# Performance work log

Measured on AMD Instinct MI355X. Metric: run time of the kernel, lower is better.

## Reference

```python
import jax, jax.numpy as jnp
import numpy as np

D = 1024  # input_dim


def setup_inputs() -> dict:
    key = jax.random.key(0)
    ks = jax.random.split(key, 7)
    s = 1.0 / np.sqrt(D)
    return {
        "x": jax.random.normal(ks[0], (4, 2048, D), dtype=jnp.float32),
        "wq": jax.random.normal(ks[1], (D, D), dtype=jnp.float32) * s,
        "bq": jax.random.normal(ks[2], (D,), dtype=jnp.float32) * s,
        "wk": jax.random.normal(ks[3], (D, D), dtype=jnp.float32) * s,
        "bk": jax.random.normal(ks[4], (D,), dtype=jnp.float32) * s,
        "wv": jax.random.normal(ks[5], (D, D), dtype=jnp.float32) * s,
        "bv": jax.random.normal(ks[6], (D,), dtype=jnp.float32) * s,
    }


def reference(x, wq, bq, wk, bk, wv, bv):
    # torch Linear: y = x @ W^T + b
    q = jnp.einsum('btd,ed->bte', x, wq) + bq  # (B,T,D)
    k = jnp.einsum('btd,ed->bte', x, wk) + bk
    v = jnp.einsum('btd,ed->bte', x, wv) + bv
    scale = 1.0 / jnp.sqrt(jnp.asarray(D, dtype=x.dtype))
    scores = jnp.einsum('btd,bsd->bts', q, k) * scale  # (B,T,T)
    attn = jax.nn.softmax(scores, axis=-1)
    return jnp.einsum('bts,bsd->btd', attn, v)
```

## Files before the change

kernel.cpp:

```cpp
#include <hip/hip_runtime.h>
#include <stdint.h>

#define BB 4
#define TT 2048
#define DD 1024

typedef unsigned short u16;
typedef unsigned int u32;
typedef u16 u16x4 __attribute__((ext_vector_type(4)));
typedef u16 u16x8 __attribute__((ext_vector_type(8)));
typedef float f32x4 __attribute__((ext_vector_type(4)));
typedef short s16x8 __attribute__((ext_vector_type(8)));

__device__ __forceinline__ u16 f2bf(float f) {
  u32 u = __float_as_uint(f);
  return (u16)((u + 0x7fffu + ((u >> 16) & 1u)) >> 16);
}
__device__ __forceinline__ float bf2f(u16 h) {
  return __uint_as_float((u32)h << 16);
}

__device__ __forceinline__ void gload_lds16(const void* g, void* l) {
  __builtin_amdgcn_global_load_lds(
      (const __attribute__((address_space(1))) u32*)g,
      (__attribute__((address_space(3))) u32*)l, 16, 0, 0);
}

__device__ __forceinline__ void swz(int BMv, int BNv, int& tileM, int& tileN) {
  const int gN = gridDim.x, gM = gridDim.y;
  const int L = blockIdx.y * gN + blockIdx.x;
  const int xcd = L & 7, j = L >> 3;
  const int Mq = gM >> 2, Nq = gN >> 1;
  tileM = (((xcd >> 1) * Mq) + j / Nq) * BMv;
  tileN = (((xcd & 1) * Nq) + j % Nq) * BNv;
}

__global__ __launch_bounds__(256) void cast_bf16_kernel(
    const float* __restrict__ in, u16* __restrict__ out, int n8) {
  int i = blockIdx.x * 256 + threadIdx.x;
  if (i >= n8) return;
  const f32x4* p = (const f32x4*)in;
  f32x4 a = p[2 * (size_t)i];
  f32x4 b = p[2 * (size_t)i + 1];
  u16x8 o;
  o[0] = f2bf(a[0]); o[1] = f2bf(a[1]); o[2] = f2bf(a[2]); o[3] = f2bf(a[3]);
  o[4] = f2bf(b[0]); o[5] = f2bf(b[1]); o[6] = f2bf(b[2]); o[7] = f2bf(b[3]);
  *(u16x8*)(out + 8 * (size_t)i) = o;
}

__global__ __launch_bounds__(256) void wcast_kernel(
    const float* __restrict__ wq, const float* __restrict__ wk,
    const float* __restrict__ wv, u16* __restrict__ out) {
  int i = blockIdx.x * 256 + threadIdx.x;
  const int n1 = DD * DD / 8;
  const float* src = i < n1 ? wq : (i < 2 * n1 ? wk : wv);
  int ii = i < n1 ? i : (i < 2 * n1 ? i - n1 : i - 2 * n1);
  const f32x4* p = (const f32x4*)src;
  f32x4 a = p[2 * (size_t)ii];
  f32x4 b = p[2 * (size_t)ii + 1];
  u16x8 o;
  o[0] = f2bf(a[0]); o[1] = f2bf(a[1]); o[2] = f2bf(a[2]); o[3] = f2bf(a[3]);
  o[4] = f2bf(b[0]); o[5] = f2bf(b[1]); o[6] = f2bf(b[2]); o[7] = f2bf(b[3]);
  *(u16x8*)(out + 8 * (size_t)i) = o;
}

__global__ __launch_bounds__(256) void bias_concat_kernel(
    const float* __restrict__ bq, const float* __restrict__ bk,
    const float* __restrict__ bv, float* __restrict__ out) {
  int i = blockIdx.x * 256 + threadIdx.x;
  float v = i < DD ? bq[i] : (i < 2 * DD ? bk[i - DD] : bv[i - 2 * DD]);
  out[i] = v;
}

template <int NR>
__device__ __forceinline__ void kloop256(
    const u16* __restrict__ A, const u16* __restrict__ B, int lda, int ldb,
    int K, int tileM, int tileN, u16* sm, f32x4 (&acc)[8][NR]) {
  constexpr int AE = 16384;
  constexpr int BUF = AE + NR * 4096;
  const int tid = threadIdx.x;
  const int lane = tid & 63;
  const int wave = tid >> 6;
  const int quad = lane >> 4;
  const int l15 = lane & 15;
  const int wm = (wave >> 2) << 7;
  const int wn = (wave & 3) * (NR * 16);

  const int chl = wave * 64 + lane;
  const int rloc = chl >> 3;
  const int cg = ((chl & 7) ^ (rloc & 7)) * 8;
  const int ldst = chl * 8;

  const u16* gA[4];
  const u16* gB[NR];
#pragma unroll
  for (int j = 0; j < 4; ++j)
    gA[j] = A + (size_t)(tileM + j * 64 + rloc) * lda + cg;
#pragma unroll
  for (int j = 0; j < NR; ++j)
    gB[j] = B + (size_t)(tileN + j * 64 + rloc) * ldb + cg;

  const int x0 = (quad ^ (l15 & 7)) * 8;
  int aOff[8];
  int bOff[NR];
#pragma unroll
  for (int i = 0; i < 8; ++i) aOff[i] = (wm + i * 16 + l15) * 64 + x0;
#pragma unroll
  for (int i = 0; i < NR; ++i) bOff[i] = AE + (wn + i * 16 + l15) * 64 + x0;

  {
    u16* d = sm;
    gload_lds16(gA[0], d + 0 * 4096 + ldst);
    gload_lds16(gA[2], d + 2 * 4096 + ldst);
#pragma unroll
    for (int j = 0; j < NR; ++j) gload_lds16(gB[j], d + AE + j * 4096 + ldst);
    gload_lds16(gA[1], d + 1 * 4096 + ldst);
    gload_lds16(gA[3], d + 3 * 4096 + ldst);
#pragma unroll
    for (int j = 0; j < 4; ++j) gA[j] += 64;
#pragma unroll
    for (int j = 0; j < NR; ++j) gB[j] += 64;
  }
  asm volatile("s_waitcnt vmcnt(2)" ::: "memory");
  __builtin_amdgcn_s_barrier();
  __builtin_amdgcn_sched_barrier(0);

  const int NT = K >> 6;
  for (int t = 0; t < NT; ++t) {
    const u16* sb = sm + (t & 1) * BUF;
    u16* st = sm + ((t + 1) & 1) * BUF;
    const bool stg = (t + 1 < NT);
    s16x8 af[4], bf[NR];

#pragma unroll
    for (int i = 0; i < 4; ++i) af[i] = *(const s16x8*)(sb + aOff[i]);
#pragma unroll
    for (int i = 0; i < NR; ++i) bf[i] = *(const s16x8*)(sb + bOff[i]);
    if (stg) {
      gload_lds16(gA[0], st + 0 * 4096 + ldst);
      gload_lds16(gA[2], st + 2 * 4096 + ldst);
    }
    __builtin_amdgcn_s_barrier();
    __builtin_amdgcn_sched_barrier(0);
    asm volatile("s_waitcnt lgkmcnt(0)" ::: "memory");
    __builtin_amdgcn_s_setprio(1);
#pragma unroll
    for (int mi = 0; mi < 4; ++mi)
#pragma unroll
      for (int ni = 0; ni < NR; ++ni)
        acc[mi][ni] = __builtin_amdgcn_mfma_f32_16x16x32_bf16(
            af[mi], bf[ni], acc[mi][ni], 0, 0, 0);
    __builtin_amdgcn_s_setprio(0);
    if (stg) {
      asm volatile("s_waitcnt vmcnt(2)" ::: "memory");
    } else {
      asm volatile("s_waitcnt vmcnt(0)" ::: "memory");
    }
    __builtin_amdgcn_s_barrier();
    __builtin_amdgcn_sched_barrier(0);

#pragma unroll
    for (int i = 0; i < 4; ++i) af[i] = *(const s16x8*)(sb + aOff[4 + i]);
    if (stg) {
      gload_lds16(gB[0], st + AE + 0 * 4096 + ldst);
      gload_lds16(gB[1], st + AE + 1 * 4096 + ldst);
    }
    __builtin_amdgcn_s_barrier();
    __builtin_amdgcn_sched_barrier(0);
    asm volatile("s_waitcnt lgkmcnt(0)" ::: "memory");
    __builtin_amdgcn_s_setprio(1);
#pragma unroll
    for (int mi = 0; mi < 4; ++mi)
#pragma unroll
      for (int ni = 0; ni < NR; ++ni)
        acc[4 + mi][ni] = __builtin_amdgcn_mfma_f32_16x16x32_bf16(
            af[mi], bf[ni], acc[4 + mi][ni], 0, 0, 0);
    __builtin_amdgcn_s_setprio(0);
    __builtin_amdgcn_s_barrier();
    __builtin_amdgcn_sched_barrier(0);

#pragma unroll
    for (int i = 0; i < 4; ++i) af[i] = *(const s16x8*)(sb + (aOff[i] ^ 32));
#pragma unroll
    for (int i = 0; i < NR; ++i) bf[i] = *(const s16x8*)(sb + (bOff[i] ^ 32));
    if (stg) {
      gload_lds16(gB[2], st + AE + 2 * 4096 + ldst);
      if constexpr (NR == 4) gload_lds16(gB[3], st + AE + 3 * 4096 + ldst);
    }
    __builtin_amdgcn_s_barrier();
    __builtin_amdgcn_sched_barrier(0);
    asm volatile("s_waitcnt lgkmcnt(0)" ::: "memory");
    __builtin_amdgcn_s_setprio(1);
#pragma unroll
    for (int mi = 0; mi < 4; ++mi)
#pragma unroll
      for (int ni = 0; ni < NR; ++ni)
        acc[mi][ni] = __builtin_amdgcn_mfma_f32_16x16x32_bf16(
            af[mi], bf[ni], acc[mi][ni], 0, 0, 0);
    __builtin_amdgcn_s_setprio(0);
    __builtin_amdgcn_s_barrier();
    __builtin_amdgcn_sched_barrier(0);

#pragma unroll
    for (int i = 0; i < 4; ++i)
      af[i] = *(const s16x8*)(sb + (aOff[4 + i] ^ 32));
    if (stg) {
      gload_lds16(gA[1], st + 1 * 4096 + ldst);
      gload_lds16(gA[3], st + 3 * 4096 + ldst);
#pragma unroll
      for (int j = 0; j < 4; ++j) gA[j] += 64;
#pragma unroll
      for (int j = 0; j < NR; ++j) gB[j] += 64;
    }
    __builtin_amdgcn_s_barrier();
    __builtin_amdgcn_sched_barrier(0);
    asm volatile("s_waitcnt lgkmcnt(0)" ::: "memory");
    __builtin_amdgcn_s_setprio(1);
#pragma unroll
    for (int mi = 0; mi < 4; ++mi)
#pragma unroll
      for (int ni = 0; ni < NR; ++ni)
        acc[4 + mi][ni] = __builtin_amdgcn_mfma_f32_16x16x32_bf16(
            af[mi], bf[ni], acc[4 + mi][ni], 0, 0, 0);
    __builtin_amdgcn_s_setprio(0);
    if (stg) asm volatile("s_waitcnt vmcnt(2)" ::: "memory");
    __builtin_amdgcn_s_barrier();
    __builtin_amdgcn_sched_barrier(0);
  }
}

__device__ __forceinline__ void kloop_bt(
    const u16* __restrict__ A, const u16* __restrict__ B, int lda, int ldb,
    int K, int tileM, int tileN, u16* sA, u16* sB, f32x4 acc[4][4]) {
  const int tid = threadIdx.x;
  const int lane = tid & 63;
  const int wave = tid >> 6;
  const int quad = lane >> 4;
  const int l15 = lane & 15;
  const int wm = (wave >> 1) << 6;
  const int wn = (wave & 1) << 6;

  const u16 *gA[4], *gB[4];
  u16 *lA[4], *lB[4];
#pragma unroll
  for (int j = 0; j < 4; ++j) {
    const int ch = wave * 256 + j * 64 + lane;
    const int r = ch >> 3;
    const int cg = ((ch & 7) ^ (r & 7)) * 8;
    gA[j] = A + (size_t)(tileM + r) * lda + cg;
    gB[j] = B + (size_t)(tileN + r) * ldb + cg;
    lA[j] = sA + wave * 2048 + j * 512;
    lB[j] = sB + wave * 2048 + j * 512;
  }

  const int x0 = (quad ^ (l15 & 7)) * 8;
  int aOff[4], bOff[4];
#pragma unroll
  for (int i = 0; i < 4; ++i) {
    aOff[i] = (wm + i * 16 + l15) * 64 + x0;
    bOff[i] = (wn + i * 16 + l15) * 64 + x0;
  }

  for (int it = 0; it < K; it += 64) {
#pragma unroll
    for (int j = 0; j < 4; ++j) gload_lds16(gA[j], lA[j]);
#pragma unroll
    for (int j = 0; j < 4; ++j) gload_lds16(gB[j], lB[j]);
#pragma unroll
    for (int j = 0; j < 4; ++j) { gA[j] += 64; gB[j] += 64; }
    __syncthreads();

    s16x8 af[4], bf[4];
#pragma unroll
    for (int i = 0; i < 4; ++i) af[i] = *(const s16x8*)(sA + aOff[i]);
#pragma unroll
    for (int i = 0; i < 4; ++i) bf[i] = *(const s16x8*)(sB + bOff[i]);
#pragma unroll
    for (int mi = 0; mi < 4; ++mi)
#pragma unroll
      for (int ni = 0; ni < 4; ++ni)
        acc[mi][ni] = __builtin_amdgcn_mfma_f32_16x16x32_bf16(
            af[mi], bf[ni], acc[mi][ni], 0, 0, 0);

#pragma unroll
    for (int i = 0; i < 4; ++i) af[i] = *(const s16x8*)(sA + (aOff[i] ^ 32));
#pragma unroll
    for (int i = 0; i < 4; ++i) bf[i] = *(const s16x8*)(sB + (bOff[i] ^ 32));
#pragma unroll
    for (int mi = 0; mi < 4; ++mi)
#pragma unroll
      for (int ni = 0; ni < 4; ++ni)
        acc[mi][ni] = __builtin_amdgcn_mfma_f32_16x16x32_bf16(
            af[mi], bf[ni], acc[mi][ni], 0, 0, 0);
    __syncthreads();
  }
}

__global__ __launch_bounds__(512, 2) void gemm_qkv(
    const u16* __restrict__ A, const u16* __restrict__ B,
    u16* __restrict__ qk, u16* __restrict__ vt, const float* __restrict__ bias) {
  __shared__ u16 sm[2 * (16384 + 3 * 4096)];
  const int lane = threadIdx.x & 63;
  const int wave = threadIdx.x >> 6;
  const int quad = lane >> 4;
  const int l15 = lane & 15;
  const int wm = (wave >> 2) << 7;
  const int wn = (wave & 3) * 48;
  int tileM, tileN;
  swz(256, 192, tileM, tileN);

  f32x4 acc[8][3] = {};
  kloop256<3>(A, B, DD, DD, DD, tileM, tileN, sm, acc);

  const int rowB = tileM + wm + quad * 4;
#pragma unroll
  for (int ni = 0; ni < 3; ++ni) {
    const int c0 = tileN + wn + ni * 16;
    const int col = c0 + l15;
    const float bs = bias[col];
    if (c0 < 2048) {
      const float scale = c0 < 1024 ? 0.03125f : 1.0f;
#pragma unroll
      for (int mi = 0; mi < 8; ++mi)
#pragma unroll
        for (int r = 0; r < 4; ++r)
          qk[(size_t)(rowB + mi * 16 + r) * 2048 + col] =
              f2bf((acc[mi][ni][r] + bs) * scale);
    } else {
      const int b = tileM >> 11;
      const int tBase = rowB & 2047;
      u16* vb = vt + (size_t)b * DD * TT + (size_t)(col - 2048) * TT;
#pragma unroll
      for (int mi = 0; mi < 8; ++mi) {
        u16x4 o;
#pragma unroll
        for (int r = 0; r < 4; ++r) o[r] = f2bf(acc[mi][ni][r] + bs);
        *(u16x4*)(vb + tBase + mi * 16) = o;
      }
    }
  }
}

__global__ __launch_bounds__(512, 2) void gemm_s(
    const u16* __restrict__ qk, u16* __restrict__ sbuf,
    float* __restrict__ part) {
  __shared__ u16 sm[2 * (16384 + 4 * 4096)];
  const int lane = threadIdx.x & 63;
  const int wave = threadIdx.x >> 6;
  const int quad = lane >> 4;
  const int l15 = lane & 15;
  const int wm = (wave >> 2) << 7;
  const int wn = (wave & 3) << 6;
  int tileM, tileN;
  swz(256, 256, tileM, tileN);
  const int z = blockIdx.z;

  const u16* A = qk + (size_t)z * TT * 2048;
  const u16* B = qk + (size_t)z * TT * 2048 + 1024;

  f32x4 acc[8][4] = {};
  kloop256<4>(A, B, 2048, 2048, 1024, tileM, tileN, sm, acc);

  const int rowB = tileM + wm + quad * 4;
  const int colB = tileN + wn + l15;
  u16* C = sbuf + (size_t)z * TT * 2048;
  const int nIdx2 = (tileN + wn) >> 6;
  float* prow = part + ((size_t)z * 32 + nIdx2) * TT;
#pragma unroll
  for (int mi = 0; mi < 8; ++mi)
#pragma unroll
    for (int r = 0; r < 4; ++r) {
      const int row = rowB + mi * 16 + r;
      u16* crow = C + (size_t)row * 2048 + colB;
      float s = 0.f;
#pragma unroll
      for (int ni = 0; ni < 4; ++ni) {
        const u16 h = f2bf(__expf(acc[mi][ni][r]));
        crow[ni * 16] = h;
        s += bf2f(h);
      }
#pragma unroll
      for (int m = 1; m <= 8; m <<= 1) s += __shfl_xor(s, m, 64);
      if (l15 == 0) prow[row] = s;
    }
}

__global__ __launch_bounds__(256, 2) void gemm_pv(
    const u16* __restrict__ sbuf, const u16* __restrict__ vt,
    float* __restrict__ out, const float* __restrict__ part) {
  __shared__ u16 sA[128 * 64];
  __shared__ u16 sB[128 * 64];
  __shared__ float rowInv[128];
  const int tid = threadIdx.x;
  const int lane = tid & 63;
  const int wave = tid >> 6;
  const int quad = lane >> 4;
  const int l15 = lane & 15;
  const int wm = (wave >> 1) << 6;
  const int wn = (wave & 1) << 6;
  int tileM, tileN;
  swz(128, 128, tileM, tileN);
  const int z = blockIdx.z;

  if (tid < 128) {
    const float* pp = part + (size_t)z * 32 * TT + tileM + tid;
    float s = 0.f;
#pragma unroll
    for (int j = 0; j < 32; ++j) s += pp[j * TT];
    rowInv[tid] = 1.0f / s;
  }

  const u16* A = sbuf + (size_t)z * TT * 2048;
  const u16* B = vt + (size_t)z * DD * TT;

  f32x4 acc[4][4] = {};
  kloop_bt(A, B, 2048, TT, TT, tileM, tileN, sA, sB, acc);

  const int rowB = tileM + wm + quad * 4;
  const int colB = tileN + wn + l15;
  float* C = out + (size_t)z * TT * DD;
#pragma unroll
  for (int mi = 0; mi < 4; ++mi)
#pragma unroll
    for (int r = 0; r < 4; ++r) {
      const int lrow = wm + quad * 4 + mi * 16 + r;
      const float inv = rowInv[lrow];
      float* crow = C + (size_t)(rowB + mi * 16 + r) * DD + colB;
#pragma unroll
      for (int ni = 0; ni < 4; ++ni) crow[ni * 16] = acc[mi][ni][r] * inv;
    }
}

extern "C" void kernel_launch(void* const* d_in, const int* in_sizes, int n_in,
                              void* d_out, int out_size, void* d_ws,
                              size_t ws_size, hipStream_t stream) {
  const float* x = (const float*)d_in[0];
  const float* wq = (const float*)d_in[1];
  const float* bq = (const float*)d_in[2];
  const float* wk = (const float*)d_in[3];
  const float* bk = (const float*)d_in[4];
  const float* wv = (const float*)d_in[5];
  const float* bv = (const float*)d_in[6];
  float* out = (float*)d_out;

  const size_t MB = 1024 * 1024;
  if (ws_size < 103 * MB) return;
  char* ws = (char*)d_ws;
  u16* xbf = (u16*)(ws);
  float* part = (float*)(ws);
  u16* wcat = (u16*)(ws + 16 * MB);
  float* bcat = (float*)(ws + 22 * MB);
  u16* qk = (u16*)(ws + 23 * MB);
  u16* vt = (u16*)(ws + 55 * MB);
  u16* sbuf = (u16*)(ws + 71 * MB);

  const dim3 blk256(256);
  const dim3 blk512(512);

  cast_bf16_kernel<<<BB * TT * DD / 8 / 256, blk256, 0, stream>>>(
      x, xbf, BB * TT * DD / 8);
  wcast_kernel<<<3 * DD * DD / 8 / 256, blk256, 0, stream>>>(wq, wk, wv, wcat);
  bias_concat_kernel<<<12, blk256, 0, stream>>>(bq, bk, bv, bcat);

  gemm_qkv<<<dim3(3 * DD / 192, BB * TT / 256, 1), blk512, 0, stream>>>(
      xbf, wcat, qk, vt, bcat);

  gemm_s<<<dim3(TT / 256, TT / 256, BB), blk512, 0, stream>>>(qk, sbuf, part);

  gemm_pv<<<dim3(DD / 128, TT / 128, BB), blk256, 0, stream>>>(
      sbuf, vt, out, part);
}
```

Before: 240.5 us.

## Front-load global-to-LDS prefetch in GEMM loop and stage QK epilogue through LDS

After: 238.1 us. Within noise of the previous version (-1.0%).

```diff
diff --git a/kernel.cpp b/kernel.cpp
--- a/kernel.cpp
+++ b/kernel.cpp
@@ -139,10 +139,13 @@
     if (stg) {
       gload_lds16(gA[0], st + 0 * 4096 + ldst);
       gload_lds16(gA[2], st + 2 * 4096 + ldst);
+      gload_lds16(gB[0], st + AE + 0 * 4096 + ldst);
+      gload_lds16(gB[1], st + AE + 1 * 4096 + ldst);
     }
     __builtin_amdgcn_s_barrier();
     __builtin_amdgcn_sched_barrier(0);
     asm volatile("s_waitcnt lgkmcnt(0)" ::: "memory");
+    __builtin_amdgcn_sched_barrier(0);
     __builtin_amdgcn_s_setprio(1);
 #pragma unroll
     for (int mi = 0; mi < 4; ++mi)
@@ -152,7 +155,7 @@
             af[mi], bf[ni], acc[mi][ni], 0, 0, 0);
     __builtin_amdgcn_s_setprio(0);
     if (stg) {
-      asm volatile("s_waitcnt vmcnt(2)" ::: "memory");
+      asm volatile("s_waitcnt vmcnt(4)" ::: "memory");
     } else {
       asm volatile("s_waitcnt vmcnt(0)" ::: "memory");
     }
@@ -162,12 +165,19 @@
 #pragma unroll
     for (int i = 0; i < 4; ++i) af[i] = *(const s16x8*)(sb + aOff[4 + i]);
     if (stg) {
-      gload_lds16(gB[0], st + AE + 0 * 4096 + ldst);
-      gload_lds16(gB[1], st + AE + 1 * 4096 + ldst);
+      if constexpr (NR >= 3) gload_lds16(gB[2], st + AE + 2 * 4096 + ldst);
+      if constexpr (NR >= 4) gload_lds16(gB[3], st + AE + 3 * 4096 + ldst);
+      gload_lds16(gA[1], st + 1 * 4096 + ldst);
+      gload_lds16(gA[3], st + 3 * 4096 + ldst);
+#pragma unroll
+      for (int j = 0; j < 4; ++j) gA[j] += 64;
+#pragma unroll
+      for (int j = 0; j < NR; ++j) gB[j] += 64;
     }
     __builtin_amdgcn_s_barrier();
     __builtin_amdgcn_sched_barrier(0);
     asm volatile("s_waitcnt lgkmcnt(0)" ::: "memory");
+    __builtin_amdgcn_sched_barrier(0);
     __builtin_amdgcn_s_setprio(1);
 #pragma unroll
     for (int mi = 0; mi < 4; ++mi)
@@ -183,13 +193,10 @@
     for (int i = 0; i < 4; ++i) af[i] = *(const s16x8*)(sb + (aOff[i] ^ 32));
 #pragma unroll
     for (int i = 0; i < NR; ++i) bf[i] = *(const s16x8*)(sb + (bOff[i] ^ 32));
-    if (stg) {
-      gload_lds16(gB[2], st + AE + 2 * 4096 + ldst);
-      if constexpr (NR == 4) gload_lds16(gB[3], st + AE + 3 * 4096 + ldst);
-    }
     __builtin_amdgcn_s_barrier();
     __builtin_amdgcn_sched_barrier(0);
     asm volatile("s_waitcnt lgkmcnt(0)" ::: "memory");
+    __builtin_amdgcn_sched_barrier(0);
     __builtin_amdgcn_s_setprio(1);
 #pragma unroll
     for (int mi = 0; mi < 4; ++mi)
@@ -204,17 +211,10 @@
 #pragma unroll
     for (int i = 0; i < 4; ++i)
       af[i] = *(const s16x8*)(sb + (aOff[4 + i] ^ 32));
-    if (stg) {
-      gload_lds16(gA[1], st + 1 * 4096 + ldst);
-      gload_lds16(gA[3], st + 3 * 4096 + ldst);
-#pragma unroll
-      for (int j = 0; j < 4; ++j) gA[j] += 64;
-#pragma unroll
-      for (int j = 0; j < NR; ++j) gB[j] += 64;
-    }
     __builtin_amdgcn_s_barrier();
     __builtin_amdgcn_sched_barrier(0);
     asm volatile("s_waitcnt lgkmcnt(0)" ::: "memory");
+    __builtin_amdgcn_sched_barrier(0);
     __builtin_amdgcn_s_setprio(1);
 #pragma unroll
     for (int mi = 0; mi < 4; ++mi)
@@ -300,8 +300,9 @@
     const u16* __restrict__ A, const u16* __restrict__ B,
     u16* __restrict__ qk, u16* __restrict__ vt, const float* __restrict__ bias) {
   __shared__ u16 sm[2 * (16384 + 3 * 4096)];
-  const int lane = threadIdx.x & 63;
-  const int wave = threadIdx.x >> 6;
+  const int tid = threadIdx.x;
+  const int lane = tid & 63;
+  const int wave = tid >> 6;
   const int quad = lane >> 4;
   const int l15 = lane & 15;
   const int wm = (wave >> 2) << 7;
@@ -312,24 +313,25 @@
   f32x4 acc[8][3] = {};
   kloop256<3>(A, B, DD, DD, DD, tileM, tileN, sm, acc);
 
-  const int rowB = tileM + wm + quad * 4;
+  constexpr int ES = 196;
+  const int rowL = wm + quad * 4;
 #pragma unroll
   for (int ni = 0; ni < 3; ++ni) {
     const int c0 = tileN + wn + ni * 16;
-    const int col = c0 + l15;
-    const float bs = bias[col];
+    const float bs = bias[c0 + l15];
     if (c0 < 2048) {
       const float scale = c0 < 1024 ? 0.03125f : 1.0f;
+      const int colL = wn + ni * 16 + l15;
 #pragma unroll
       for (int mi = 0; mi < 8; ++mi)
 #pragma unroll
         for (int r = 0; r < 4; ++r)
-          qk[(size_t)(rowB + mi * 16 + r) * 2048 + col] =
+          sm[(rowL + mi * 16 + r) * ES + colL] =
               f2bf((acc[mi][ni][r] + bs) * scale);
     } else {
       const int b = tileM >> 11;
-      const int tBase = rowB & 2047;
-      u16* vb = vt + (size_t)b * DD * TT + (size_t)(col - 2048) * TT;
+      const int tBase = (tileM + rowL) & 2047;
+      u16* vb = vt + (size_t)b * DD * TT + (size_t)(c0 + l15 - 2048) * TT;
 #pragma unroll
       for (int mi = 0; mi < 8; ++mi) {
         u16x4 o;
@@ -337,6 +339,19 @@
         for (int r = 0; r < 4; ++r) o[r] = f2bf(acc[mi][ni][r] + bs);
         *(u16x4*)(vb + tBase + mi * 16) = o;
       }
+    }
+  }
+  __syncthreads();
+  if (tileN < 2048) {
+    const int row = tid >> 1;
+    const int cb = (tid & 1) * 12;
+    u16* grow = qk + (size_t)(tileM + row) * 2048 + tileN;
+    const u16* lrow = sm + row * ES;
+#pragma unroll
+    for (int j = 0; j < 12; ++j) {
+      const int c = cb + j;
+      if (tileN + c * 8 < 2048)
+        *(u16x8*)(grow + c * 8) = *(const u16x8*)(lrow + c * 8);
     }
   }
 }
```

## Switch QKV GEMM to 128x128 tiles and front-load kloop256 prefetches

Applied to the files above, without the earlier changes.

Result: no change. 236.4 us (-1.7%).

```diff
diff --git a/kernel.cpp b/kernel.cpp
--- a/kernel.cpp
+++ b/kernel.cpp
@@ -139,10 +139,13 @@
     if (stg) {
       gload_lds16(gA[0], st + 0 * 4096 + ldst);
       gload_lds16(gA[2], st + 2 * 4096 + ldst);
+      gload_lds16(gB[0], st + AE + 0 * 4096 + ldst);
+      gload_lds16(gB[1], st + AE + 1 * 4096 + ldst);
     }
     __builtin_amdgcn_s_barrier();
     __builtin_amdgcn_sched_barrier(0);
     asm volatile("s_waitcnt lgkmcnt(0)" ::: "memory");
+    __builtin_amdgcn_sched_barrier(0);
     __builtin_amdgcn_s_setprio(1);
 #pragma unroll
     for (int mi = 0; mi < 4; ++mi)
@@ -152,7 +155,7 @@
             af[mi], bf[ni], acc[mi][ni], 0, 0, 0);
     __builtin_amdgcn_s_setprio(0);
     if (stg) {
-      asm volatile("s_waitcnt vmcnt(2)" ::: "memory");
+      asm volatile("s_waitcnt vmcnt(4)" ::: "memory");
     } else {
       asm volatile("s_waitcnt vmcnt(0)" ::: "memory");
     }
@@ -162,12 +165,19 @@
 #pragma unroll
     for (int i = 0; i < 4; ++i) af[i] = *(const s16x8*)(sb + aOff[4 + i]);
     if (stg) {
-      gload_lds16(gB[0], st + AE + 0 * 4096 + ldst);
-      gload_lds16(gB[1], st + AE + 1 * 4096 + ldst);
+      if constexpr (NR >= 3) gload_lds16(gB[2], st + AE + 2 * 4096 + ldst);
+      if constexpr (NR >= 4) gload_lds16(gB[3], st + AE + 3 * 4096 + ldst);
+      gload_lds16(gA[1], st + 1 * 4096 + ldst);
+      gload_lds16(gA[3], st + 3 * 4096 + ldst);
+#pragma unroll
+      for (int j = 0; j < 4; ++j) gA[j] += 64;
+#pragma unroll
+      for (int j = 0; j < NR; ++j) gB[j] += 64;
     }
     __builtin_amdgcn_s_barrier();
     __builtin_amdgcn_sched_barrier(0);
     asm volatile("s_waitcnt lgkmcnt(0)" ::: "memory");
+    __builtin_amdgcn_sched_barrier(0);
     __builtin_amdgcn_s_setprio(1);
 #pragma unroll
     for (int mi = 0; mi < 4; ++mi)
@@ -183,13 +193,10 @@
     for (int i = 0; i < 4; ++i) af[i] = *(const s16x8*)(sb + (aOff[i] ^ 32));
 #pragma unroll
     for (int i = 0; i < NR; ++i) bf[i] = *(const s16x8*)(sb + (bOff[i] ^ 32));
-    if (stg) {
-      gload_lds16(gB[2], st + AE + 2 * 4096 + ldst);
-      if constexpr (NR == 4) gload_lds16(gB[3], st + AE + 3 * 4096 + ldst);
-    }
     __builtin_amdgcn_s_barrier();
     __builtin_amdgcn_sched_barrier(0);
     asm volatile("s_waitcnt lgkmcnt(0)" ::: "memory");
+    __builtin_amdgcn_sched_barrier(0);
     __builtin_amdgcn_s_setprio(1);
 #pragma unroll
     for (int mi = 0; mi < 4; ++mi)
@@ -204,17 +211,10 @@
 #pragma unroll
     for (int i = 0; i < 4; ++i)
       af[i] = *(const s16x8*)(sb + (aOff[4 + i] ^ 32));
-    if (stg) {
-      gload_lds16(gA[1], st + 1 * 4096 + ldst);
-      gload_lds16(gA[3], st + 3 * 4096 + ldst);
-#pragma unroll
-      for (int j = 0; j < 4; ++j) gA[j] += 64;
-#pragma unroll
-      for (int j = 0; j < NR; ++j) gB[j] += 64;
-    }
     __builtin_amdgcn_s_barrier();
     __builtin_amdgcn_sched_barrier(0);
     asm volatile("s_waitcnt lgkmcnt(0)" ::: "memory");
+    __builtin_amdgcn_sched_barrier(0);
     __builtin_amdgcn_s_setprio(1);
 #pragma unroll
     for (int mi = 0; mi < 4; ++mi)
@@ -296,48 +296,51 @@
   }
 }
 
-__global__ __launch_bounds__(512, 2) void gemm_qkv(
+__global__ __launch_bounds__(256, 2) void gemm_qkv(
     const u16* __restrict__ A, const u16* __restrict__ B,
     u16* __restrict__ qk, u16* __restrict__ vt, const float* __restrict__ bias) {
-  __shared__ u16 sm[2 * (16384 + 3 * 4096)];
+  __shared__ u16 sA[128 * 64];
+  __shared__ u16 sB[128 * 64];
   const int lane = threadIdx.x & 63;
   const int wave = threadIdx.x >> 6;
   const int quad = lane >> 4;
   const int l15 = lane & 15;
-  const int wm = (wave >> 2) << 7;
-  const int wn = (wave & 3) * 48;
+  const int wm = (wave >> 1) << 6;
+  const int wn = (wave & 1) << 6;
   int tileM, tileN;
-  swz(256, 192, tileM, tileN);
-
-  f32x4 acc[8][3] = {};
-  kloop256<3>(A, B, DD, DD, DD, tileM, tileN, sm, acc);
+  swz(128, 128, tileM, tileN);
+
+  f32x4 acc[4][4] = {};
+  kloop_bt(A, B, DD, DD, DD, tileM, tileN, sA, sB, acc);
 
   const int rowB = tileM + wm + quad * 4;
-#pragma unroll
-  for (int ni = 0; ni < 3; ++ni) {
-    const int c0 = tileN + wn + ni * 16;
-    const int col = c0 + l15;
-    const float bs = bias[col];
-    if (c0 < 2048) {
-      const float scale = c0 < 1024 ? 0.03125f : 1.0f;
-#pragma unroll
-      for (int mi = 0; mi < 8; ++mi)
-#pragma unroll
-        for (int r = 0; r < 4; ++r)
-          qk[(size_t)(rowB + mi * 16 + r) * 2048 + col] =
-              f2bf((acc[mi][ni][r] + bs) * scale);
-    } else {
-      const int b = tileM >> 11;
-      const int tBase = rowB & 2047;
-      u16* vb = vt + (size_t)b * DD * TT + (size_t)(col - 2048) * TT;
-#pragma unroll
-      for (int mi = 0; mi < 8; ++mi) {
+  const int colB = tileN + wn + l15;
+  if (tileN < 2048) {
+    const float scale = (tileN < 1024) ? 0.03125f : 1.0f;
+#pragma unroll
+    for (int mi = 0; mi < 4; ++mi)
+#pragma unroll
+      for (int r = 0; r < 4; ++r) {
+        u16* crow = qk + (size_t)(rowB + mi * 16 + r) * 2048 + colB;
+#pragma unroll
+        for (int ni = 0; ni < 4; ++ni)
+          crow[ni * 16] = f2bf((acc[mi][ni][r] + bias[colB + ni * 16]) * scale);
+      }
+  } else {
+    const int b = tileM >> 11;
+    const int tBase = (rowB & 2047);
+    u16* vb = vt + (size_t)b * DD * TT;
+#pragma unroll
+    for (int mi = 0; mi < 4; ++mi)
+#pragma unroll
+      for (int ni = 0; ni < 4; ++ni) {
+        const int e = colB + ni * 16 - 2048;
+        const float bs = bias[colB + ni * 16];
         u16x4 o;
 #pragma unroll
         for (int r = 0; r < 4; ++r) o[r] = f2bf(acc[mi][ni][r] + bs);
-        *(u16x4*)(vb + tBase + mi * 16) = o;
+        *(u16x4*)(vb + (size_t)e * TT + tBase + mi * 16) = o;
       }
-    }
   }
 }
 
@@ -462,7 +465,7 @@
   wcast_kernel<<<3 * DD * DD / 8 / 256, blk256, 0, stream>>>(wq, wk, wv, wcat);
   bias_concat_kernel<<<12, blk256, 0, stream>>>(bq, bk, bv, bcat);
 
-  gemm_qkv<<<dim3(3 * DD / 192, BB * TT / 256, 1), blk512, 0, stream>>>(
+  gemm_qkv<<<dim3(3 * DD / 128, BB * TT / 128, 1), blk256, 0, stream>>>(
       xbf, wcat, qk, vt, bcat);
 
   gemm_s<<<dim3(TT / 256, TT / 256, BB), blk512, 0, stream>>>(qk, sbuf, part);
```
